# Kernel optimization log

Measured on AMD Instinct MI355X. Metric: run time of the kernel, lower is better.

Reference implementation:

```python
import jax, jax.numpy as jnp
import numpy as np

EPS = 1e-7
K_IN, K_HID, K_OUT = 1.0, 1.1, 1.2
N_NODES, N_EDGES, IN_DIM, HID = 50000, 400000, 1024, 1024


def _expmap0(u, k):
    # u: tangent at origin with time component 0; u[:, 1:] are spatial coords
    sqrtK = jnp.sqrt(k)
    us = u[:, 1:]
    un = jnp.maximum(jnp.linalg.norm(us, axis=1, keepdims=True), EPS)
    t = un / sqrtK
    return jnp.concatenate([sqrtK * jnp.cosh(t), sqrtK * jnp.sinh(t) * us / un], axis=1)


def _logmap0(x, k):
    sqrtK = jnp.sqrt(k)
    x0, xs = x[:, 0:1], x[:, 1:]
    xn = jnp.maximum(jnp.linalg.norm(xs, axis=1, keepdims=True), EPS)
    theta = jnp.maximum(x0 / sqrtK, 1.0 + EPS)
    d = sqrtK * jnp.arccosh(theta)
    return jnp.concatenate([jnp.zeros_like(x0), d * xs / xn], axis=1)


def _proj(x, k):
    # re-fix the time component so <x,x>_L = -k
    xs = x[:, 1:]
    x0 = jnp.sqrt(k + jnp.sum(xs * xs, axis=1, keepdims=True))
    return jnp.concatenate([x0, xs], axis=1)


def _centroid(m, k):
    # Lorentzian centroid normalization: sqrt(k) * m / sqrt(|<m,m>_L|)
    l_inner = jnp.sum(m[:, 1:] ** 2, axis=1, keepdims=True) - m[:, 0:1] ** 2
    denom = jnp.sqrt(jnp.maximum(jnp.abs(l_inner), EPS))
    return jnp.sqrt(k) * m / denom


def _lgcn_conv(x, W, b, edge_src, edge_dst, edge_w, k_in, k_out):
    n = x.shape[0]
    # Lorentzian linear: logmap0 -> spatial matmul + bias -> expmap0
    u = _logmap0(x, k_in)[:, 1:]                      # [N, in_f]
    mx = u @ W.T + b                                  # [N, out_f-1]
    h = _expmap0(jnp.concatenate([jnp.zeros_like(mx[:, :1]), mx], axis=1), k_in)
    # sparse neighborhood aggregation + Lorentzian centroid
    msgs = edge_w[:, None] * h[edge_src]              # [E, out_f]
    m = jax.ops.segment_sum(msgs, edge_dst, num_segments=n)
    h = _centroid(m, k_in)
    # Lorentzian activation: relu in tangent space, re-exp on output manifold
    t = jax.nn.relu(_logmap0(h, k_in))                # time comp stays 0
    return _proj(_expmap0(t, k_out), k_out)


def setup_inputs() -> dict:
    key = jax.random.key(0)
    ks = jax.random.split(key, 8)
    x = jax.random.normal(ks[0], (N_NODES, IN_DIM), jnp.float32) * 0.01
    edge_src = jax.random.randint(ks[1], (N_EDGES,), 0, N_NODES, jnp.int32)
    edge_dst = jax.random.randint(ks[2], (N_EDGES,), 0, N_NODES, jnp.int32)
    edge_w = jax.random.uniform(ks[3], (N_EDGES,), jnp.float32)
    W1 = jax.random.normal(ks[4], (HID - 1, IN_DIM), jnp.float32) * 0.02
    b1 = jax.random.normal(ks[5], (HID - 1,), jnp.float32) * 0.01
    W2 = jax.random.normal(ks[6], (HID - 1, HID - 1), jnp.float32) * 0.02
    b2 = jax.random.normal(ks[7], (HID - 1,), jnp.float32) * 0.01
    return {"x": x, "edge_src": edge_src, "edge_dst": edge_dst, "edge_w": edge_w,
            "W1": W1, "b1": b1, "W2": W2, "b2": b2}


def reference(x, edge_src, edge_dst, edge_w, W1, b1, W2, b2):
    # encode(): prepend zero time coord, proj_tan0 (already 0), expmap0, proj
    x = jnp.concatenate([jnp.zeros_like(x[:, :1]), x], axis=1)  # [N, IN_DIM+1]
    xh = _proj(_expmap0(x, K_IN), K_IN)
    x1 = _lgcn_conv(xh, W1, b1, edge_src, edge_dst, edge_w, K_IN, K_HID)
    y = _lgcn_conv(x1, W2, b2, edge_src, edge_dst, edge_w, K_HID, K_OUT)
    return y
```

## Files before the change

kernel.cpp:

```cpp
#include <hip/hip_runtime.h>
#include <math.h>

#define EPSF 1e-7f
#define KPAD 1024
#define M_PAD 50048
#define NBM 391
#define NWG (NBM * 8)

typedef __attribute__((ext_vector_type(8))) short bf16x8;
typedef __attribute__((ext_vector_type(4))) float f32x4;
typedef __attribute__((ext_vector_type(4))) unsigned short us4;
typedef __attribute__((ext_vector_type(8))) unsigned short us8;

__device__ inline unsigned short f2bf(float f) {
  unsigned u = __float_as_uint(f);
  return (unsigned short)((u + 0x7FFFu + ((u >> 16) & 1u)) >> 16);
}
__device__ inline float bf2f(unsigned short s) {
  return __uint_as_float(((unsigned)s) << 16);
}

__device__ inline float block_sum256(float v, float* s4) {
#pragma unroll
  for (int o = 32; o > 0; o >>= 1) v += __shfl_down(v, o);
  int lane = threadIdx.x & 63, w = threadIdx.x >> 6;
  __syncthreads();
  if (lane == 0) s4[w] = v;
  __syncthreads();
  return s4[0] + s4[1] + s4[2] + s4[3];
}

__device__ inline void gload_lds16(const void* g, void* l) {
  __builtin_amdgcn_global_load_lds((const __attribute__((address_space(1))) void*)g,
                                   (__attribute__((address_space(3))) void*)l, 16, 0, 0);
}

__global__ __launch_bounds__(256) void cvt_rows_bf16(const float* __restrict__ x,
                                                     unsigned short* __restrict__ o) {
  int i = blockIdx.x, t = threadIdx.x;
  float4 v = *(const float4*)(x + (size_t)i * 1024 + 4 * t);
  us4 u = {f2bf(v.x), f2bf(v.y), f2bf(v.z), f2bf(v.w)};
  *(us4*)(o + (size_t)i * 1024 + 4 * t) = u;
}

__global__ __launch_bounds__(256) void cvt_w_bf16(const float* __restrict__ W,
                                                  unsigned short* __restrict__ o,
                                                  int rows, int cols) {
  int r = blockIdx.x, t = threadIdx.x;
  int c0 = 4 * t;
  us4 u;
#pragma unroll
  for (int j = 0; j < 4; ++j) {
    int c = c0 + j;
    float v = (r < rows && c < cols) ? W[(size_t)r * cols + c] : 0.0f;
    u[j] = f2bf(v);
  }
  *(us4*)(o + (size_t)r * 1024 + c0) = u;
}

__global__ __launch_bounds__(256) void gemm_bt(const unsigned short* __restrict__ A,
                                               const unsigned short* __restrict__ B,
                                               const float* __restrict__ bias,
                                               unsigned short* __restrict__ C) {
  __shared__ unsigned short lA[2][128 * 32];
  __shared__ unsigned short lB[2][128 * 32];
  const int wg = blockIdx.x;
  const int swz = (wg & 7) * NBM + (wg >> 3);
  const int bm = swz >> 3, bn = swz & 7;
  const int tid = threadIdx.x;
  const int wave = tid >> 6, lane = tid & 63;
  const int wr = wave >> 1, wc = wave & 1;
  const int fr = lane & 15, fg = lane >> 4;

  f32x4 acc[4][4];
#pragma unroll
  for (int m = 0; m < 4; ++m)
#pragma unroll
    for (int n2 = 0; n2 < 4; ++n2) acc[m][n2] = (f32x4)0.0f;

  for (int k0 = 0; k0 < KPAD; k0 += 64) {
#pragma unroll
    for (int h = 0; h < 2; ++h) {
#pragma unroll
      for (int q = 0; q < 2; ++q) {
        int row = q * 64 + wave * 16 + (lane >> 2);
        int kk = ((lane & 3) ^ ((row >> 1) & 3)) << 3;
        gload_lds16(A + (size_t)(bm * 128 + row) * KPAD + k0 + h * 32 + kk,
                    &lA[h][row * 32 + ((lane & 3) << 3)]);
        gload_lds16(B + (size_t)(bn * 128 + row) * KPAD + k0 + h * 32 + kk,
                    &lB[h][row * 32 + ((lane & 3) << 3)]);
      }
    }
    __syncthreads();
#pragma unroll
    for (int h = 0; h < 2; ++h) {
      bf16x8 a[4], b[4];
#pragma unroll
      for (int m = 0; m < 4; ++m) {
        int row = wr * 64 + m * 16 + fr;
        a[m] = *(const bf16x8*)&lA[h][row * 32 + ((fg ^ ((row >> 1) & 3)) << 3)];
      }
#pragma unroll
      for (int n2 = 0; n2 < 4; ++n2) {
        int row = wc * 64 + n2 * 16 + fr;
        b[n2] = *(const bf16x8*)&lB[h][row * 32 + ((fg ^ ((row >> 1) & 3)) << 3)];
      }
#pragma unroll
      for (int m = 0; m < 4; ++m)
#pragma unroll
        for (int n2 = 0; n2 < 4; ++n2)
          acc[m][n2] = __builtin_amdgcn_mfma_f32_16x16x32_bf16(a[m], b[n2], acc[m][n2], 0, 0, 0);
    }
    __syncthreads();
  }

  const int crow0 = bm * 128 + wr * 64;
  const int ccol0 = bn * 128 + wc * 64;
#pragma unroll
  for (int m = 0; m < 4; ++m) {
#pragma unroll
    for (int n2 = 0; n2 < 4; ++n2) {
      int col = ccol0 + n2 * 16 + fr;
      float bv = (col < 1023) ? bias[col] : 0.0f;
      int row0 = crow0 + m * 16 + fg * 4;
      unsigned short* cp = C + (size_t)row0 * 1024 + col;
#pragma unroll
      for (int j = 0; j < 4; ++j) cp[(size_t)j * 1024] = f2bf(acc[m][n2][j] + bv);
    }
  }
}

__global__ __launch_bounds__(256) void row_scale(unsigned short* __restrict__ raw,
                                                 float* __restrict__ sc_tab, float sqrtK) {
  __shared__ float s4[4];
  int i = blockIdx.x, t = threadIdx.x;
  const us4 v = *(const us4*)(raw + (size_t)i * 1024 + 4 * t);
  float f0 = bf2f(v[0]), f1 = bf2f(v[1]), f2 = bf2f(v[2]), f3 = bf2f(v[3]);
  if (t == 255) f3 = 0.0f;
  float ss = block_sum256(f0 * f0 + f1 * f1 + f2 * f2 + f3 * f3, s4);
  float un = fmaxf(sqrtf(ss), EPSF);
  float tt = un / sqrtK;
  float e = expf(tt);
  float ch = 0.5f * (e + 1.0f / e), sh = 0.5f * (e - 1.0f / e);
  float h0 = sqrtK * ch, sc = sqrtK * sh / un;
  if (t == 0) sc_tab[i] = sc;
  if (t == 255) raw[(size_t)i * 1024 + 1023] = f2bf(h0 / sc);
}

__global__ __launch_bounds__(256) void deg_count(const int* __restrict__ ed, int* __restrict__ cnt,
                                                 int nE) {
  int i = blockIdx.x * 256 + threadIdx.x;
  if (i < nE) atomicAdd(&cnt[ed[i]], 1);
}

__global__ __launch_bounds__(256) void scan1(const int* __restrict__ cnt, int* __restrict__ excl,
                                             int* __restrict__ bsum, int n) {
  __shared__ int s[256];
  int t = threadIdx.x;
  int i = blockIdx.x * 256 + t;
  int v = (i < n) ? cnt[i] : 0;
  s[t] = v;
  __syncthreads();
#pragma unroll
  for (int o = 1; o < 256; o <<= 1) {
    int add = (t >= o) ? s[t - o] : 0;
    __syncthreads();
    s[t] += add;
    __syncthreads();
  }
  if (i < n) excl[i] = s[t] - v;
  if (t == 255) bsum[blockIdx.x] = s[t];
}

__global__ __launch_bounds__(256) void scan2(int* __restrict__ bsum, int* __restrict__ boff,
                                             int nb) {
  __shared__ int s[256];
  int t = threadIdx.x;
  int v = (t < nb) ? bsum[t] : 0;
  s[t] = v;
  __syncthreads();
#pragma unroll
  for (int o = 1; o < 256; o <<= 1) {
    int add = (t >= o) ? s[t - o] : 0;
    __syncthreads();
    s[t] += add;
    __syncthreads();
  }
  if (t < nb) boff[t] = s[t] - v;
}

__global__ __launch_bounds__(256) void scan3(int* __restrict__ excl, const int* __restrict__ boff,
                                             int* __restrict__ rowstart, int* __restrict__ fill,
                                             int n, int nE) {
  int i = blockIdx.x * 256 + threadIdx.x;
  if (i < n) {
    int v = excl[i] + boff[blockIdx.x];
    rowstart[i] = v;
    fill[i] = v;
  }
  if (i == 0) rowstart[n] = nE;
}

__global__ __launch_bounds__(256) void bucket_fill(const int* __restrict__ es,
                                                   const int* __restrict__ ed,
                                                   const float* __restrict__ ew,
                                                   int* __restrict__ fill,
                                                   int2* __restrict__ sedge, int nE) {
  int i = blockIdx.x * 256 + threadIdx.x;
  if (i < nE) {
    int d = ed[i];
    int pos = atomicAdd(&fill[d], 1);
    sedge[pos] = make_int2(es[i], __float_as_int(ew[i]));
  }
}

__device__ inline void gather_row(const unsigned short* __restrict__ h,
                                  const float* __restrict__ sc,
                                  const int2* __restrict__ sedge, int j0, int j1, int t,
                                  float* acc) {
  int j = j0;
  for (; j + 4 <= j1; j += 4) {
    int2 e0 = sedge[j], e1 = sedge[j + 1], e2 = sedge[j + 2], e3 = sedge[j + 3];
    float w0 = __int_as_float(e0.y) * sc[e0.x];
    float w1 = __int_as_float(e1.y) * sc[e1.x];
    float w2 = __int_as_float(e2.y) * sc[e2.x];
    float w3 = __int_as_float(e3.y) * sc[e3.x];
    us8 v0 = *(const us8*)(h + (size_t)e0.x * 1024 + 8 * t);
    us8 v1 = *(const us8*)(h + (size_t)e1.x * 1024 + 8 * t);
    us8 v2 = *(const us8*)(h + (size_t)e2.x * 1024 + 8 * t);
    us8 v3 = *(const us8*)(h + (size_t)e3.x * 1024 + 8 * t);
#pragma unroll
    for (int q = 0; q < 8; ++q) {
      acc[q] += w0 * bf2f(v0[q]);
      acc[q] += w1 * bf2f(v1[q]);
      acc[q] += w2 * bf2f(v2[q]);
      acc[q] += w3 * bf2f(v3[q]);
    }
  }
  for (; j < j1; ++j) {
    int2 e = sedge[j];
    float w = __int_as_float(e.y) * sc[e.x];
    us8 v = *(const us8*)(h + (size_t)e.x * 1024 + 8 * t);
#pragma unroll
    for (int q = 0; q < 8; ++q) acc[q] += w * bf2f(v[q]);
  }
}

__global__ __launch_bounds__(256) void gather_centroid_tangent(
    const unsigned short* __restrict__ h, const float* __restrict__ sc,
    const int* __restrict__ rs, const int2* __restrict__ sedge,
    unsigned short* __restrict__ u16, float sqrtK, int n) {
  __shared__ float s4[4];
  __shared__ float sm0[2];
  int g = threadIdx.x >> 7;
  int t = threadIdx.x & 127;
  int i = blockIdx.x * 2 + g;
  bool alive = (i < n);
  int j0 = alive ? rs[i] : 0, j1 = alive ? rs[i + 1] : 0;
  float acc[8] = {0.f, 0.f, 0.f, 0.f, 0.f, 0.f, 0.f, 0.f};
  gather_row(h, sc, sedge, j0, j1, t, acc);
  if (t == 127) sm0[g] = acc[7];
  __syncthreads();
  float m0 = sm0[g];
  if (t == 127) acc[7] = 0.0f;
  float ssl = 0.f;
#pragma unroll
  for (int q = 0; q < 8; ++q) ssl += acc[q] * acc[q];
#pragma unroll
  for (int o = 32; o > 0; o >>= 1) ssl += __shfl_down(ssl, o);
  int lane = threadIdx.x & 63, wv = threadIdx.x >> 6;
  if (lane == 0) s4[wv] = ssl;
  __syncthreads();
  float ss = s4[2 * g] + s4[2 * g + 1];

  float l = ss - m0 * m0;
  float denom = sqrtf(fmaxf(fabsf(l), EPSF));
  float c = sqrtK / denom;
  float xn = fmaxf(c * sqrtf(ss), EPSF);
  float theta = fmaxf(m0 / denom, 1.0f + EPSF);
  float d = sqrtK * acoshf(theta);
  float f = c * (d / xn);
  us8 u;
#pragma unroll
  for (int q = 0; q < 8; ++q) u[q] = f2bf(fmaxf(acc[q], 0.0f) * f);
  if (t == 127) u[7] = 0;
  if (alive) *(us8*)(u16 + (size_t)i * 1024 + 8 * t) = u;
}

__global__ __launch_bounds__(256) void gather_centroid_final(
    const unsigned short* __restrict__ h, const float* __restrict__ sc,
    const int* __restrict__ rs, const int2* __restrict__ sedge, float* __restrict__ y,
    float sqrtKin, float sqrtKout, int n) {
  __shared__ float s4[4];
  __shared__ float s4b[4];
  __shared__ float sm0[2];
  int g = threadIdx.x >> 7;
  int t = threadIdx.x & 127;
  int i = blockIdx.x * 2 + g;
  bool alive = (i < n);
  int j0 = alive ? rs[i] : 0, j1 = alive ? rs[i + 1] : 0;
  float acc[8] = {0.f, 0.f, 0.f, 0.f, 0.f, 0.f, 0.f, 0.f};
  gather_row(h, sc, sedge, j0, j1, t, acc);
  if (t == 127) sm0[g] = acc[7];
  __syncthreads();
  float m0 = sm0[g];
  if (t == 127) acc[7] = 0.0f;
  float ssl = 0.f;
#pragma unroll
  for (int q = 0; q < 8; ++q) ssl += acc[q] * acc[q];
#pragma unroll
  for (int o = 32; o > 0; o >>= 1) ssl += __shfl_down(ssl, o);
  int lane = threadIdx.x & 63, wv = threadIdx.x >> 6;
  if (lane == 0) s4[wv] = ssl;
  __syncthreads();
  float ss = s4[2 * g] + s4[2 * g + 1];

  float l = ss - m0 * m0;
  float denom = sqrtf(fmaxf(fabsf(l), EPSF));
  float c = sqrtKin / denom;
  float xn = fmaxf(c * sqrtf(ss), EPSF);
  float theta = fmaxf(m0 / denom, 1.0f + EPSF);
  float d = sqrtKin * acoshf(theta);
  float f = c * (d / xn);
  float o_[8];
#pragma unroll
  for (int q = 0; q < 8; ++q) o_[q] = fmaxf(acc[q], 0.0f) * f;
  if (t == 127) o_[7] = 0.0f;
  float ss2l = 0.f;
#pragma unroll
  for (int q = 0; q < 8; ++q) ss2l += o_[q] * o_[q];
#pragma unroll
  for (int o = 32; o > 0; o >>= 1) ss2l += __shfl_down(ss2l, o);
  if (lane == 0) s4b[wv] = ss2l;
  __syncthreads();
  float ss2 = s4b[2 * g] + s4b[2 * g + 1];

  float un = fmaxf(sqrtf(ss2), EPSF);
  float tt = un / sqrtKout;
  float e = expf(tt);
  float ch = 0.5f * (e + 1.0f / e), sh = 0.5f * (e - 1.0f / e);
  float y0 = sqrtKout * ch, scale = sqrtKout * sh / un;
  if (alive) {
    float* yr = y + (size_t)i * 1024;
    int c0 = 8 * t;
#pragma unroll
    for (int q = 0; q < 8; ++q) {
      int col = c0 + q;
      if (col < 1023) yr[1 + col] = scale * o_[q];
    }
    if (t == 0) yr[0] = y0;
  }
}

extern "C" void kernel_launch(void* const* d_in, const int* in_sizes, int n_in,
                              void* d_out, int out_size, void* d_ws, size_t ws_size,
                              hipStream_t stream) {
  const float* x = (const float*)d_in[0];
  const int* es = (const int*)d_in[1];
  const int* ed = (const int*)d_in[2];
  const float* ew = (const float*)d_in[3];
  const float* W1 = (const float*)d_in[4];
  const float* b1 = (const float*)d_in[5];
  const float* W2 = (const float*)d_in[6];
  const float* b2 = (const float*)d_in[7];
  float* y = (float*)d_out;

  const int n = in_sizes[0] / 1024;
  const int nE = in_sizes[1];
  const int NB = (n + 255) / 256;
  const int EB = (nE + 255) / 256;

  char* ws = (char*)d_ws;
  size_t off = 0;
  auto alloc = [&](size_t bytes) {
    void* p = ws + off;
    off += (bytes + 255) & ~(size_t)255;
    return p;
  };
  unsigned short* u16 = (unsigned short*)alloc((size_t)M_PAD * 1024 * 2);
  unsigned short* w16 = (unsigned short*)alloc((size_t)1024 * 1024 * 2);
  unsigned short* raw16 = (unsigned short*)alloc((size_t)M_PAD * 1024 * 2);
  float* sc_tab = (float*)alloc((size_t)M_PAD * 4);
  int* cnt = (int*)alloc((size_t)(n + 1) * 4);
  int* excl = (int*)alloc((size_t)n * 4);
  int* rowstart = (int*)alloc((size_t)(n + 1) * 4);
  int* fill = (int*)alloc((size_t)n * 4);
  int* bsum = (int*)alloc(256 * 4);
  int* boff = (int*)alloc(256 * 4);
  int2* sedge = (int2*)alloc((size_t)nE * 8);

  const float sK1 = 1.0f;
  const float sK2 = 1.0488088481701516f;
  const float sK3 = 1.0954451150103321f;

  const int GB = (n + 1) / 2;

  hipMemsetAsync(cnt, 0, (size_t)(n + 1) * 4, stream);
  deg_count<<<EB, 256, 0, stream>>>(ed, cnt, nE);
  scan1<<<NB, 256, 0, stream>>>(cnt, excl, bsum, n);
  scan2<<<1, 256, 0, stream>>>(bsum, boff, NB);
  scan3<<<NB, 256, 0, stream>>>(excl, boff, rowstart, fill, n, nE);
  bucket_fill<<<EB, 256, 0, stream>>>(es, ed, ew, fill, sedge, nE);

  cvt_rows_bf16<<<n, 256, 0, stream>>>(x, u16);
  cvt_w_bf16<<<1024, 256, 0, stream>>>(W1, w16, 1023, 1024);
  gemm_bt<<<NWG, 256, 0, stream>>>(u16, w16, b1, raw16);
  row_scale<<<n, 256, 0, stream>>>(raw16, sc_tab, sK1);
  gather_centroid_tangent<<<GB, 256, 0, stream>>>(raw16, sc_tab, rowstart, sedge, u16, sK1, n);

  cvt_w_bf16<<<1024, 256, 0, stream>>>(W2, w16, 1023, 1023);
  gemm_bt<<<NWG, 256, 0, stream>>>(u16, w16, b2, raw16);
  row_scale<<<n, 256, 0, stream>>>(raw16, sc_tab, sK2);
  gather_centroid_final<<<GB, 256, 0, stream>>>(raw16, sc_tab, rowstart, sedge, y, sK2, sK3, n);
}
```

Before: 718.6 us.

## Use 256x256 GEMM tiles with 4-stage LDS pipeline and simplify gather tail

Replaces the 128x128 double-phase GEMM with a 256x256-tile, 512-thread kernel that keeps a four-deep ring of LDS buffers and overlaps global-to-LDS loads with MFMA compute through manual vmcnt waits and a single barrier per k-step. It also raises MFMA priority during compute. The gather loop drops its scalar tail and instead pads the last group of four edges with zero weights. The larger tiles cut global traffic per FLOP, but they raise register and LDS pressure, which can lower occupancy, and they need M padded to 50176, so the allocation must match.

```diff
diff --git a/kernel.cpp b/kernel.cpp
--- a/kernel.cpp
+++ b/kernel.cpp
@@ -3,9 +3,8 @@
 
 #define EPSF 1e-7f
 #define KPAD 1024
-#define M_PAD 50048
-#define NBM 391
-#define NWG (NBM * 8)
+#define M_PAD 50176
+#define NWG2 784
 
 typedef __attribute__((ext_vector_type(8))) short bf16x8;
 typedef __attribute__((ext_vector_type(4))) float f32x4;
@@ -58,66 +57,88 @@
   *(us4*)(o + (size_t)r * 1024 + c0) = u;
 }
 
-__global__ __launch_bounds__(256) void gemm_bt(const unsigned short* __restrict__ A,
-                                               const unsigned short* __restrict__ B,
-                                               const float* __restrict__ bias,
-                                               unsigned short* __restrict__ C) {
-  __shared__ unsigned short lA[2][128 * 32];
-  __shared__ unsigned short lB[2][128 * 32];
+__global__ __launch_bounds__(512, 2) void gemm_bt256(const unsigned short* __restrict__ A,
+                                                     const unsigned short* __restrict__ B,
+                                                     const float* __restrict__ bias,
+                                                     unsigned short* __restrict__ C) {
+  __shared__ unsigned short lA[4][256 * 32];
+  __shared__ unsigned short lB[4][256 * 32];
   const int wg = blockIdx.x;
-  const int swz = (wg & 7) * NBM + (wg >> 3);
-  const int bm = swz >> 3, bn = swz & 7;
+  const int swz = (wg & 7) * 98 + (wg >> 3);
+  const int bm = swz >> 2, bn = swz & 3;
   const int tid = threadIdx.x;
   const int wave = tid >> 6, lane = tid & 63;
-  const int wr = wave >> 1, wc = wave & 1;
+  const int wr = wave >> 2, wc = wave & 3;
   const int fr = lane & 15, fg = lane >> 4;
-
-  f32x4 acc[4][4];
-#pragma unroll
-  for (int m = 0; m < 4; ++m)
+  const int srow = tid >> 2;
+  const int sg = tid & 3;
+
+  const unsigned short* Abase = A + (size_t)bm * 256 * KPAD;
+  const unsigned short* Bbase = B + (size_t)bn * 256 * KPAD;
+
+  f32x4 acc[8][4];
+#pragma unroll
+  for (int m = 0; m < 8; ++m)
 #pragma unroll
     for (int n2 = 0; n2 < 4; ++n2) acc[m][n2] = (f32x4)0.0f;
 
-  for (int k0 = 0; k0 < KPAD; k0 += 64) {
-#pragma unroll
-    for (int h = 0; h < 2; ++h) {
-#pragma unroll
-      for (int q = 0; q < 2; ++q) {
-        int row = q * 64 + wave * 16 + (lane >> 2);
-        int kk = ((lane & 3) ^ ((row >> 1) & 3)) << 3;
-        gload_lds16(A + (size_t)(bm * 128 + row) * KPAD + k0 + h * 32 + kk,
-                    &lA[h][row * 32 + ((lane & 3) << 3)]);
-        gload_lds16(B + (size_t)(bn * 128 + row) * KPAD + k0 + h * 32 + kk,
-                    &lB[h][row * 32 + ((lane & 3) << 3)]);
-      }
-    }
-    __syncthreads();
-#pragma unroll
-    for (int h = 0; h < 2; ++h) {
-      bf16x8 a[4], b[4];
-#pragma unroll
-      for (int m = 0; m < 4; ++m) {
-        int row = wr * 64 + m * 16 + fr;
-        a[m] = *(const bf16x8*)&lA[h][row * 32 + ((fg ^ ((row >> 1) & 3)) << 3)];
-      }
-#pragma unroll
-      for (int n2 = 0; n2 < 4; ++n2) {
-        int row = wc * 64 + n2 * 16 + fr;
-        b[n2] = *(const bf16x8*)&lB[h][row * 32 + ((fg ^ ((row >> 1) & 3)) << 3)];
-      }
-#pragma unroll
-      for (int m = 0; m < 4; ++m)
-#pragma unroll
-        for (int n2 = 0; n2 < 4; ++n2)
-          acc[m][n2] = __builtin_amdgcn_mfma_f32_16x16x32_bf16(a[m], b[n2], acc[m][n2], 0, 0, 0);
-    }
-    __syncthreads();
-  }
-
-  const int crow0 = bm * 128 + wr * 64;
-  const int ccol0 = bn * 128 + wc * 64;
-#pragma unroll
-  for (int m = 0; m < 4; ++m) {
+  auto STAGE = [&](int t) {
+    const int k0 = t * 32;
+    const int buf = t & 3;
+#pragma unroll
+    for (int q = 0; q < 2; ++q) {
+      int row = q * 128 + srow;
+      int ksrc = k0 + ((sg ^ ((row >> 1) & 3)) << 3);
+      gload_lds16(Abase + (size_t)row * KPAD + ksrc, &lA[buf][row * 32 + (sg << 3)]);
+      gload_lds16(Bbase + (size_t)row * KPAD + ksrc, &lB[buf][row * 32 + (sg << 3)]);
+    }
+  };
+
+  auto COMPUTE = [&](int t) {
+    const int buf = t & 3;
+    bf16x8 a[8], b[4];
+#pragma unroll
+    for (int m = 0; m < 8; ++m) {
+      int row = wr * 128 + m * 16 + fr;
+      a[m] = *(const bf16x8*)&lA[buf][row * 32 + ((fg ^ ((row >> 1) & 3)) << 3)];
+    }
+#pragma unroll
+    for (int n2 = 0; n2 < 4; ++n2) {
+      int row = wc * 64 + n2 * 16 + fr;
+      b[n2] = *(const bf16x8*)&lB[buf][row * 32 + ((fg ^ ((row >> 1) & 3)) << 3)];
+    }
+    __builtin_amdgcn_s_setprio(1);
+#pragma unroll
+    for (int m = 0; m < 8; ++m)
+#pragma unroll
+      for (int n2 = 0; n2 < 4; ++n2)
+        acc[m][n2] = __builtin_amdgcn_mfma_f32_16x16x32_bf16(a[m], b[n2], acc[m][n2], 0, 0, 0);
+    __builtin_amdgcn_s_setprio(0);
+  };
+
+  STAGE(0);
+  STAGE(1);
+  STAGE(2);
+  for (int t = 0; t < 29; ++t) {
+    asm volatile("s_waitcnt vmcnt(8)" ::: "memory");
+    __builtin_amdgcn_s_barrier();
+    STAGE(t + 3);
+    COMPUTE(t);
+  }
+  asm volatile("s_waitcnt vmcnt(8)" ::: "memory");
+  __builtin_amdgcn_s_barrier();
+  COMPUTE(29);
+  asm volatile("s_waitcnt vmcnt(4)" ::: "memory");
+  __builtin_amdgcn_s_barrier();
+  COMPUTE(30);
+  asm volatile("s_waitcnt vmcnt(0)" ::: "memory");
+  __builtin_amdgcn_s_barrier();
+  COMPUTE(31);
+
+  const int crow0 = bm * 256 + wr * 128;
+  const int ccol0 = bn * 256 + wc * 64;
+#pragma unroll
+  for (int m = 0; m < 8; ++m) {
 #pragma unroll
     for (int n2 = 0; n2 < 4; ++n2) {
       int col = ccol0 + n2 * 16 + fr;
@@ -218,31 +239,27 @@
                                   const float* __restrict__ sc,
                                   const int2* __restrict__ sedge, int j0, int j1, int t,
                                   float* acc) {
-  int j = j0;
-  for (; j + 4 <= j1; j += 4) {
-    int2 e0 = sedge[j], e1 = sedge[j + 1], e2 = sedge[j + 2], e3 = sedge[j + 3];
-    float w0 = __int_as_float(e0.y) * sc[e0.x];
-    float w1 = __int_as_float(e1.y) * sc[e1.x];
-    float w2 = __int_as_float(e2.y) * sc[e2.x];
-    float w3 = __int_as_float(e3.y) * sc[e3.x];
-    us8 v0 = *(const us8*)(h + (size_t)e0.x * 1024 + 8 * t);
-    us8 v1 = *(const us8*)(h + (size_t)e1.x * 1024 + 8 * t);
-    us8 v2 = *(const us8*)(h + (size_t)e2.x * 1024 + 8 * t);
-    us8 v3 = *(const us8*)(h + (size_t)e3.x * 1024 + 8 * t);
+  for (int j = j0; j < j1; j += 4) {
+    int2 e[4];
+    float w[4];
+#pragma unroll
+    for (int kk = 0; kk < 4; ++kk) {
+      int jj = j + kk;
+      int jc = (jj < j1) ? jj : (j1 - 1);
+      e[kk] = sedge[jc];
+      w[kk] = (jj < j1) ? __int_as_float(e[kk].y) * sc[e[kk].x] : 0.0f;
+    }
+    us8 v0 = *(const us8*)(h + (size_t)e[0].x * 1024 + 8 * t);
+    us8 v1 = *(const us8*)(h + (size_t)e[1].x * 1024 + 8 * t);
+    us8 v2 = *(const us8*)(h + (size_t)e[2].x * 1024 + 8 * t);
+    us8 v3 = *(const us8*)(h + (size_t)e[3].x * 1024 + 8 * t);
 #pragma unroll
     for (int q = 0; q < 8; ++q) {
-      acc[q] += w0 * bf2f(v0[q]);
-      acc[q] += w1 * bf2f(v1[q]);
-      acc[q] += w2 * bf2f(v2[q]);
-      acc[q] += w3 * bf2f(v3[q]);
-    }
-  }
-  for (; j < j1; ++j) {
-    int2 e = sedge[j];
-    float w = __int_as_float(e.y) * sc[e.x];
-    us8 v = *(const us8*)(h + (size_t)e.x * 1024 + 8 * t);
-#pragma unroll
-    for (int q = 0; q < 8; ++q) acc[q] += w * bf2f(v[q]);
+      acc[q] += w[0] * bf2f(v0[q]);
+      acc[q] += w[1] * bf2f(v1[q]);
+      acc[q] += w[2] * bf2f(v2[q]);
+      acc[q] += w[3] * bf2f(v3[q]);
+    }
   }
 }
 
@@ -404,12 +421,12 @@
 
   cvt_rows_bf16<<<n, 256, 0, stream>>>(x, u16);
   cvt_w_bf16<<<1024, 256, 0, stream>>>(W1, w16, 1023, 1024);
-  gemm_bt<<<NWG, 256, 0, stream>>>(u16, w16, b1, raw16);
+  gemm_bt256<<<NWG2, 512, 0, stream>>>(u16, w16, b1, raw16);
   row_scale<<<n, 256, 0, stream>>>(raw16, sc_tab, sK1);
   gather_centroid_tangent<<<GB, 256, 0, stream>>>(raw16, sc_tab, rowstart, sedge, u16, sK1, n);
 
   cvt_w_bf16<<<1024, 256, 0, stream>>>(W2, w16, 1023, 1023);
-  gemm_bt<<<NWG, 256, 0, stream>>>(u16, w16, b2, raw16);
+  gemm_bt256<<<NWG2, 512, 0, stream>>>(u16, w16, b2, raw16);
   row_scale<<<n, 256, 0, stream>>>(raw16, sc_tab, sK2);
   gather_centroid_final<<<GB, 256, 0, stream>>>(raw16, sc_tab, rowstart, sedge, y, sK2, sK3, n);
 }
```

New measurement: 815.7 us. 13.5% more time.

## Replace 128x128 GEMM with 256x256 tile, 8-wave software-pipelined kernel

Applied to the files above, without the earlier changes.

Replaces the bf16 GEMM with a 256x256-tile kernel using 512 threads (8 waves). It double-buffers LDS with prefetch of the next K-tiles interleaved between MFMA quadrants, using explicit vmcnt waits, barriers and s_setprio. A new XOR LDS swizzle and a reworked workgroup swizzle come with it. The goal is more data reuse per tile and overlap of global loads with compute. M padding grows to 50176, which adds wasted rows, and the larger tile raises register and LDS pressure.

```diff
diff --git a/kernel.cpp b/kernel.cpp
--- a/kernel.cpp
+++ b/kernel.cpp
@@ -3,9 +3,8 @@
 
 #define EPSF 1e-7f
 #define KPAD 1024
-#define M_PAD 50048
-#define NBM 391
-#define NWG (NBM * 8)
+#define M_PAD 50176
+#define NWG2 784
 
 typedef __attribute__((ext_vector_type(8))) short bf16x8;
 typedef __attribute__((ext_vector_type(4))) float f32x4;
@@ -58,66 +57,136 @@
   *(us4*)(o + (size_t)r * 1024 + c0) = u;
 }
 
-__global__ __launch_bounds__(256) void gemm_bt(const unsigned short* __restrict__ A,
-                                               const unsigned short* __restrict__ B,
-                                               const float* __restrict__ bias,
-                                               unsigned short* __restrict__ C) {
-  __shared__ unsigned short lA[2][128 * 32];
-  __shared__ unsigned short lB[2][128 * 32];
+__global__ __launch_bounds__(512, 2) void gemm_bt256(const unsigned short* __restrict__ A,
+                                                     const unsigned short* __restrict__ B,
+                                                     const float* __restrict__ bias,
+                                                     unsigned short* __restrict__ C) {
+  __shared__ unsigned short lA[2 * 2 * 8192];
+  __shared__ unsigned short lB[2 * 2 * 8192];
   const int wg = blockIdx.x;
-  const int swz = (wg & 7) * NBM + (wg >> 3);
-  const int bm = swz >> 3, bn = swz & 7;
+  const int swz = (wg & 7) * 98 + (wg >> 3);
+  const int bm = swz >> 2, bn = swz & 3;
   const int tid = threadIdx.x;
   const int wave = tid >> 6, lane = tid & 63;
-  const int wr = wave >> 1, wc = wave & 1;
+  const int wr = wave >> 2, wc = wave & 3;
   const int fr = lane & 15, fg = lane >> 4;
 
-  f32x4 acc[4][4];
-#pragma unroll
-  for (int m = 0; m < 4; ++m)
+  const unsigned short* Abase = A + (size_t)bm * 256 * KPAD;
+  const unsigned short* Bbase = B + (size_t)bn * 256 * KPAD;
+
+  const int aHalf = wr * 8192;
+  const int bHalf = (wc >> 1) * 8192;
+  const int lrB0 = (wc & 1) * 64;
+  int ps[2];
+#pragma unroll
+  for (int s = 0; s < 2; ++s) ps[s] = (((s << 2) + fg) ^ (fr & 7)) << 3;
+
+  const int sRow8 = lane >> 3;
+  const int sDst = wave * 512 + lane * 8;
+  const int sGran = ((lane & 7) ^ sRow8) << 3;
+
+  f32x4 acc[8][4];
+#pragma unroll
+  for (int m = 0; m < 8; ++m)
 #pragma unroll
     for (int n2 = 0; n2 < 4; ++n2) acc[m][n2] = (f32x4)0.0f;
 
-  for (int k0 = 0; k0 < KPAD; k0 += 64) {
-#pragma unroll
-    for (int h = 0; h < 2; ++h) {
-#pragma unroll
-      for (int q = 0; q < 2; ++q) {
-        int row = q * 64 + wave * 16 + (lane >> 2);
-        int kk = ((lane & 3) ^ ((row >> 1) & 3)) << 3;
-        gload_lds16(A + (size_t)(bm * 128 + row) * KPAD + k0 + h * 32 + kk,
-                    &lA[h][row * 32 + ((lane & 3) << 3)]);
-        gload_lds16(B + (size_t)(bn * 128 + row) * KPAD + k0 + h * 32 + kk,
-                    &lB[h][row * 32 + ((lane & 3) << 3)]);
-      }
-    }
-    __syncthreads();
-#pragma unroll
-    for (int h = 0; h < 2; ++h) {
-      bf16x8 a[4], b[4];
-#pragma unroll
-      for (int m = 0; m < 4; ++m) {
-        int row = wr * 64 + m * 16 + fr;
-        a[m] = *(const bf16x8*)&lA[h][row * 32 + ((fg ^ ((row >> 1) & 3)) << 3)];
-      }
-#pragma unroll
-      for (int n2 = 0; n2 < 4; ++n2) {
-        int row = wc * 64 + n2 * 16 + fr;
-        b[n2] = *(const bf16x8*)&lB[h][row * 32 + ((fg ^ ((row >> 1) & 3)) << 3)];
-      }
-#pragma unroll
-      for (int m = 0; m < 4; ++m)
-#pragma unroll
-        for (int n2 = 0; n2 < 4; ++n2)
-          acc[m][n2] = __builtin_amdgcn_mfma_f32_16x16x32_bf16(a[m], b[n2], acc[m][n2], 0, 0, 0);
-    }
-    __syncthreads();
-  }
-
-  const int crow0 = bm * 128 + wr * 64;
-  const int ccol0 = bn * 128 + wc * 64;
-#pragma unroll
-  for (int m = 0; m < 4; ++m) {
+  bf16x8 af[4][2], bf[4][2];
+
+  auto STAGE_A = [&](int t, int h) {
+    const int p = t & 1;
+#pragma unroll
+    for (int q = 0; q < 2; ++q) {
+      int row = h * 128 + q * 64 + wave * 8 + sRow8;
+      gload_lds16(Abase + (size_t)row * KPAD + t * 64 + sGran,
+                  &lA[p * 16384 + h * 8192 + q * 4096 + sDst]);
+    }
+  };
+  auto STAGE_B = [&](int t, int h) {
+    const int p = t & 1;
+#pragma unroll
+    for (int q = 0; q < 2; ++q) {
+      int row = h * 128 + q * 64 + wave * 8 + sRow8;
+      gload_lds16(Bbase + (size_t)row * KPAD + t * 64 + sGran,
+                  &lB[p * 16384 + h * 8192 + q * 4096 + sDst]);
+    }
+  };
+  auto LDA4 = [&](int p, int mg) {
+#pragma unroll
+    for (int mi = 0; mi < 4; ++mi) {
+      int ro = p * 16384 + aHalf + ((mg * 4 + mi) * 16 + fr) * 64;
+#pragma unroll
+      for (int s = 0; s < 2; ++s) af[mi][s] = *(const bf16x8*)&lA[ro + ps[s]];
+    }
+  };
+  auto LDB2 = [&](int p, int ng) {
+#pragma unroll
+    for (int ni = 0; ni < 2; ++ni) {
+      int ro = p * 16384 + bHalf + (lrB0 + (ng * 2 + ni) * 16 + fr) * 64;
+#pragma unroll
+      for (int s = 0; s < 2; ++s) bf[ng * 2 + ni][s] = *(const bf16x8*)&lB[ro + ps[s]];
+    }
+  };
+  auto MM = [&](int mq, int nq) {
+    __builtin_amdgcn_s_setprio(1);
+#pragma unroll
+    for (int mi = 0; mi < 4; ++mi)
+#pragma unroll
+      for (int ni = 0; ni < 2; ++ni)
+#pragma unroll
+        for (int s = 0; s < 2; ++s)
+          acc[mq * 4 + mi][nq * 2 + ni] = __builtin_amdgcn_mfma_f32_16x16x32_bf16(
+              af[mi][s], bf[nq * 2 + ni][s], acc[mq * 4 + mi][nq * 2 + ni], 0, 0, 0);
+    __builtin_amdgcn_s_setprio(0);
+  };
+#define BAR() __builtin_amdgcn_s_barrier()
+
+  STAGE_B(0, 0); STAGE_B(0, 1); STAGE_A(0, 0); STAGE_A(0, 1);
+  STAGE_B(1, 0); STAGE_B(1, 1); STAGE_A(1, 0);
+  asm volatile("s_waitcnt vmcnt(6)" ::: "memory");
+  BAR();
+
+#pragma unroll 1
+  for (int it = 0; it < 7; ++it) {
+    const int t0 = 2 * it, t1 = t0 + 1;
+    LDA4(0, 0); LDB2(0, 0);
+    STAGE_A(t1, 1);
+    BAR(); MM(0, 0); BAR();
+    LDB2(0, 1);
+    BAR(); MM(0, 1); BAR();
+    LDA4(0, 1);
+    STAGE_B(t0 + 2, 0);
+    BAR(); MM(1, 0); BAR();
+    STAGE_B(t0 + 2, 1); STAGE_A(t0 + 2, 0);
+    asm volatile("s_waitcnt vmcnt(6)" ::: "memory");
+    BAR(); MM(1, 1); BAR();
+    LDA4(1, 0); LDB2(1, 0);
+    STAGE_A(t0 + 2, 1);
+    BAR(); MM(0, 0); BAR();
+    LDB2(1, 1);
+    BAR(); MM(0, 1); BAR();
+    LDA4(1, 1);
+    STAGE_B(t1 + 2, 0);
+    BAR(); MM(1, 0); BAR();
+    STAGE_B(t1 + 2, 1); STAGE_A(t1 + 2, 0);
+    asm volatile("s_waitcnt vmcnt(6)" ::: "memory");
+    BAR(); MM(1, 1); BAR();
+  }
+
+  asm volatile("s_waitcnt vmcnt(0)" ::: "memory");
+  BAR();
+#pragma unroll
+  for (int p = 0; p < 2; ++p) {
+    LDA4(p, 0); LDB2(p, 0); MM(0, 0);
+    LDB2(p, 1); MM(0, 1);
+    LDA4(p, 1); MM(1, 0); MM(1, 1);
+  }
+#undef BAR
+
+  const int crow0 = bm * 256 + wr * 128;
+  const int ccol0 = bn * 256 + wc * 64;
+#pragma unroll
+  for (int m = 0; m < 8; ++m) {
 #pragma unroll
     for (int n2 = 0; n2 < 4; ++n2) {
       int col = ccol0 + n2 * 16 + fr;
@@ -404,12 +473,12 @@
 
   cvt_rows_bf16<<<n, 256, 0, stream>>>(x, u16);
   cvt_w_bf16<<<1024, 256, 0, stream>>>(W1, w16, 1023, 1024);
-  gemm_bt<<<NWG, 256, 0, stream>>>(u16, w16, b1, raw16);
+  gemm_bt256<<<NWG2, 512, 0, stream>>>(u16, w16, b1, raw16);
   row_scale<<<n, 256, 0, stream>>>(raw16, sc_tab, sK1);
   gather_centroid_tangent<<<GB, 256, 0, stream>>>(raw16, sc_tab, rowstart, sedge, u16, sK1, n);
 
   cvt_w_bf16<<<1024, 256, 0, stream>>>(W2, w16, 1023, 1023);
-  gemm_bt<<<NWG, 256, 0, stream>>>(u16, w16, b2, raw16);
+  gemm_bt256<<<NWG2, 512, 0, stream>>>(u16, w16, b2, raw16);
   row_scale<<<n, 256, 0, stream>>>(raw16, sc_tab, sK2);
   gather_centroid_final<<<GB, 256, 0, stream>>>(raw16, sc_tab, rowstart, sedge, y, sK2, sK3, n);
 }
```

Result: no change. 715.6 us (-0.4%).
